# Optimization experiments

Measured on AMD Instinct MI355X. Metric: run time of the kernel, lower is better.

Reference implementation:

```python
import jax, jax.numpy as jnp
import numpy as np

B, N = 2, 1024
DIM, HEADS, DH, MLP = 768, 12, 64, 3072
PD = 768          # channels * patch_size^2 = 3*16*16
GRID = 16         # image_size // patch_size
DEPTH = 8
INNER = HEADS * DH


def layer_norm(x, g):
    # torch F.layer_norm with beta=0 buffer, eps=1e-5
    m = x.mean(-1, keepdims=True)
    v = ((x - m) ** 2).mean(-1, keepdims=True)
    return (x - m) / jnp.sqrt(v + 1e-5) * g


def qk_rmsnorm(x, g):
    # F.normalize(x, dim=-1) * sqrt(DH) * gamma ; gamma is [H,1,DH]
    n = jnp.linalg.norm(x, axis=-1, keepdims=True)
    return x / jnp.maximum(n, 1e-12) * (DH ** 0.5) * g


def setup_inputs() -> dict:
    key = jax.random.key(0)
    ks = jax.random.split(key, 16)
    s = 0.02
    d = {
        "patches": jax.random.normal(ks[0], (B, N, PD), dtype=jnp.float32),
        "h_idx": jax.random.randint(ks[1], (B, N), 0, GRID),
        "w_idx": jax.random.randint(ks[2], (B, N), 0, GRID),
        "image_ids": jnp.sort(jax.random.randint(ks[3], (B, N), 0, 8), axis=-1),
        "pos_h": jax.random.normal(ks[4], (GRID, PD)) * s,
        "pos_w": jax.random.normal(ks[5], (GRID, PD)) * s,
        "Wp": jax.random.normal(ks[6], (PD, DIM)) * s,
        "bp": jnp.zeros((DIM,)),
        "ln_p": jnp.ones((DIM,)),
        "ln1": jnp.ones((DEPTH, DIM)),
        "qg": jnp.ones((DEPTH, HEADS, 1, DH)),
        "kg": jnp.ones((DEPTH, HEADS, 1, DH)),
        "Wq": jax.random.normal(ks[7], (DEPTH, DIM, INNER)) * s,
        "Wkv": jax.random.normal(ks[8], (DEPTH, DIM, 2 * INNER)) * s,
        "Wo": jax.random.normal(ks[9], (DEPTH, INNER, DIM)) * s,
        "ln2": jnp.ones((DEPTH, DIM)),
        "W1": jax.random.normal(ks[10], (DEPTH, DIM, MLP)) * s,
        "b1": jnp.zeros((DEPTH, MLP)),
        "W2": jax.random.normal(ks[11], (DEPTH, MLP, DIM)) * s,
        "b2": jnp.zeros((DEPTH, DIM)),
        "lnf": jnp.ones((DIM,)),
    }
    return d


def reference(patches, h_idx, w_idx, image_ids, pos_h, pos_w, Wp, bp, ln_p,
              ln1, qg, kg, Wq, Wkv, Wo, ln2, W1, b1, W2, b2, lnf):
    # pos embed added to raw patches before projection (pos_embed_before_proj=True)
    x = patches + pos_h[h_idx] + pos_w[w_idx]            # [B,N,PD]
    x = layer_norm(x @ Wp + bp, ln_p)                    # [B,N,DIM]

    # block-diagonal attn_mask: tokens attend only within their own packed image
    mask = image_ids[:, None, :, None] == image_ids[:, None, None, :]  # [B,1,N,N]

    for i in range(DEPTH):
        xn = layer_norm(x, ln1[i])
        q = (xn @ Wq[i]).reshape(B, N, HEADS, DH).transpose(0, 2, 1, 3)
        k, v = jnp.split(xn @ Wkv[i], 2, axis=-1)
        k = k.reshape(B, N, HEADS, DH).transpose(0, 2, 1, 3)
        v = v.reshape(B, N, HEADS, DH).transpose(0, 2, 1, 3)
        q = qk_rmsnorm(q, qg[i])
        k = qk_rmsnorm(k, kg[i])
        dots = jnp.einsum('bhid,bhjd->bhij', q, k)       # [B,H,N,N]
        dots = jnp.where(mask, dots, -jnp.finfo(dots.dtype).max)
        attn = jax.nn.softmax(dots, axis=-1)
        o = jnp.einsum('bhij,bhjd->bhid', attn, v)
        o = o.transpose(0, 2, 1, 3).reshape(B, N, INNER)
        x = o @ Wo[i] + x
        h = jax.nn.gelu(layer_norm(x, ln2[i]) @ W1[i] + b1[i], approximate=False)
        x = (h @ W2[i] + b2[i]) + x
    return layer_norm(x, lnf)
```

## Files before the change

### kernel.cpp

```cpp
#include <hip/hip_runtime.h>
#include <hip/hip_bf16.h>
#include <math.h>

typedef _Float16 f16;
typedef f16   f16x8 __attribute__((ext_vector_type(8)));
typedef float f32x4 __attribute__((ext_vector_type(4)));
typedef unsigned short ushort_t;

#define DIM   768
#define HEADS 12
#define DH    64
#define MLP_  3072
#define NTOK  2048
#define SEQ   1024
#define WELTS 7077888

__device__ __forceinline__ ushort_t h2u(f16 h){ return __builtin_bit_cast(ushort_t, h); }
__device__ __forceinline__ unsigned pk2h(float a, float b){
  return (unsigned)h2u((f16)a) | ((unsigned)h2u((f16)b) << 16);
}
__device__ __forceinline__ void gload16(const void* g, void* l){
  __builtin_amdgcn_global_load_lds(
      (const __attribute__((address_space(1))) void*)g,
      (__attribute__((address_space(3))) void*)l, 16, 0, 0);
}
__device__ __forceinline__ float wred_sum(float v){
  #pragma unroll
  for (int o = 32; o > 0; o >>= 1) v += __shfl_xor(v, o);
  return v;
}

__global__ __launch_bounds__(256) void convert_w_kernel(
    const float* __restrict__ Wq, const float* __restrict__ Wkv,
    const float* __restrict__ Wo, const float* __restrict__ W1,
    const float* __restrict__ W2, int layer, int wp_only,
    f16* __restrict__ th)
{
  int bid = blockIdx.x;
  const float* src; int K, N; size_t ooff; int t;
  if (wp_only){ src = Wq; K = 768; N = 768; ooff = 0; t = bid; }
  else if (bid < 288) { src = Wq;  K = 768;  N = 768;  ooff = 0;       t = bid; }
  else if (bid < 864) { src = Wkv; K = 768;  N = 1536; ooff = 589824;  t = bid - 288; }
  else if (bid < 1152){ src = Wo;  K = 768;  N = 768;  ooff = 1769472; t = bid - 864; }
  else if (bid < 2304){ src = W1;  K = 768;  N = 3072; ooff = 2359296; t = bid - 1152; }
  else                { src = W2;  K = 3072; N = 768;  ooff = 4718592; t = bid - 2304; }
  if (!wp_only) src += (size_t)layer * K * N;
  int ntn = N >> 6;
  int tk = t / ntn, tn = t % ntn;
  int k0 = tk * 32, n0 = tn * 64;

  __shared__ ushort_t lh[32][66];
  int tid = threadIdx.x;
  #pragma unroll
  for (int rr = 0; rr < 2; rr++){
    int k = rr * 16 + (tid >> 4);
    int n = (tid & 15) * 4;
    float4 v = *(const float4*)(src + (size_t)(k0 + k) * N + n0 + n);
    lh[k][n+0] = h2u((f16)v.x); lh[k][n+1] = h2u((f16)v.y);
    lh[k][n+2] = h2u((f16)v.z); lh[k][n+3] = h2u((f16)v.w);
  }
  __syncthreads();
  int n = tid >> 2, kq = tid & 3;
  unsigned ph[4];
  #pragma unroll
  for (int j = 0; j < 4; j++)
    ph[j] = (unsigned)lh[kq*8 + 2*j][n] | ((unsigned)lh[kq*8 + 2*j + 1][n] << 16);
  size_t obase = ooff + (size_t)(n0 + n) * K + k0 + kq * 8;
  *(uint4*)(th + obase) = make_uint4(ph[0], ph[1], ph[2], ph[3]);
}

__global__ __launch_bounds__(256) void gemm_big(
    const f16* __restrict__ Aq, const f16* __restrict__ Bw,
    const float* __restrict__ bias,
    float* __restrict__ C, f16* __restrict__ Cq,
    f16* __restrict__ Qh, f16* __restrict__ Kt, f16* __restrict__ Vt,
    const float* __restrict__ qgam, const float* __restrict__ kgam,
    int N, int K, int nbx, int mode)
{
  __shared__ __align__(16) f16 sA[128 * 64];
  __shared__ __align__(16) f16 sB[128 * 64];
  const int tid = threadIdx.x;
  const int wid = tid >> 6, lane = tid & 63;
  const int nwg = nbx << 4;
  const int bid = blockIdx.x;
  const int swz = (bid & 7) * (nwg >> 3) + (bid >> 3);
  const int by = swz & 15, bx = swz >> 4;
  const int brow = by << 7, bcol = bx << 7;
  const int m2 = wid & 1, n2 = wid >> 1;
  const int fr = lane & 15, fq = lane >> 4;
  const int Kc = K / (int)gridDim.z;
  const int kbase = (int)blockIdx.z * Kc;
  const int nk = Kc >> 6;

  const f16* pA = Aq + (size_t)brow * K + kbase;
  const f16* pB = Bw + (size_t)bcol * K + kbase;

  f32x4 acc[4][4] = {};

  for (int ks = 0; ks < nk; ks++){
    const int k0 = ks << 6;
    if (ks) __syncthreads();
    #pragma unroll
    for (int i = 0; i < 4; i++){
      int idx = tid + i * 256;
      int r = idx >> 3, c = idx & 7;
      int gc = c ^ (r & 7);
      gload16(pA + (size_t)r * K + k0 + gc * 8, &sA[idx * 8]);
      gload16(pB + (size_t)r * K + k0 + gc * 8, &sB[idx * 8]);
    }
    __syncthreads();
    #pragma unroll
    for (int s = 0; s < 2; s++){
      f16x8 a[4], b[4];
      #pragma unroll
      for (int m = 0; m < 4; m++){
        int r = m2 * 64 + m * 16 + fr;
        int ch = (s * 4 + fq) ^ (r & 7);
        a[m] = *(const f16x8*)(&sA[r * 64 + ch * 8]);
      }
      #pragma unroll
      for (int n = 0; n < 4; n++){
        int r = n2 * 64 + n * 16 + fr;
        int ch = (s * 4 + fq) ^ (r & 7);
        b[n] = *(const f16x8*)(&sB[r * 64 + ch * 8]);
      }
      #pragma unroll
      for (int m = 0; m < 4; m++)
        #pragma unroll
        for (int n = 0; n < 4; n++)
          acc[m][n] = __builtin_amdgcn_mfma_f32_16x16x32_f16(a[m], b[n], acc[m][n], 0, 0, 0);
    }
  }

  if (mode == 2){
    const int hbase = bcol + n2 * 64;
    if (hbase < 768){
      float gp[4];
      #pragma unroll
      for (int n = 0; n < 4; n++){
        int col = hbase + n * 16 + fr;
        gp[n] = qgam[col] * kgam[col];
      }
      #pragma unroll
      for (int m = 0; m < 4; m++)
        #pragma unroll
        for (int i = 0; i < 4; i++){
          float s = 0.f;
          #pragma unroll
          for (int n = 0; n < 4; n++) s += acc[m][n][i] * acc[m][n][i];
          s += __shfl_xor(s, 1); s += __shfl_xor(s, 2);
          s += __shfl_xor(s, 4); s += __shfl_xor(s, 8);
          float f = 8.f / fmaxf(sqrtf(s), 1e-12f);
          int row = brow + m2 * 64 + m * 16 + (fq << 2) + i;
          #pragma unroll
          for (int n = 0; n < 4; n++)
            Qh[(size_t)row * 768 + hbase + n * 16 + fr] = (f16)(acc[m][n][i] * f * gp[n]);
        }
    } else if (hbase < 1536){
      int hh = (hbase - 768) >> 6;
      #pragma unroll
      for (int m = 0; m < 4; m++)
        #pragma unroll
        for (int i = 0; i < 4; i++){
          float s = 0.f;
          #pragma unroll
          for (int n = 0; n < 4; n++) s += acc[m][n][i] * acc[m][n][i];
          s += __shfl_xor(s, 1); s += __shfl_xor(s, 2);
          s += __shfl_xor(s, 4); s += __shfl_xor(s, 8);
          float f = 8.f / fmaxf(sqrtf(s), 1e-12f);
          int row = brow + m2 * 64 + m * 16 + (fq << 2) + i;
          int bq = row >> 10, tok = row & 1023;
          #pragma unroll
          for (int n = 0; n < 4; n++)
            Kt[((size_t)(bq * 12 + hh) * 1024 + tok) * 64 + n * 16 + fr]
                = (f16)(acc[m][n][i] * f);
        }
    } else {
      int hh = (hbase - 1536) >> 6;
      #pragma unroll
      for (int n = 0; n < 4; n++){
        int dd = n * 16 + fr;
        #pragma unroll
        for (int m = 0; m < 4; m++){
          int row0 = brow + m2 * 64 + m * 16 + (fq << 2);
          int bq = row0 >> 10, tok0 = row0 & 1023;
          ushort4 sv;
          sv.x = h2u((f16)acc[m][n][0]); sv.y = h2u((f16)acc[m][n][1]);
          sv.z = h2u((f16)acc[m][n][2]); sv.w = h2u((f16)acc[m][n][3]);
          *(ushort4*)(Vt + ((size_t)((bq * 12 + hh) * 64 + dd)) * 1024 + tok0) = sv;
        }
      }
    }
  } else if (mode == 1){
    #pragma unroll
    for (int n = 0; n < 4; n++){
      int col = bcol + n2 * 64 + n * 16 + fr;
      float bv = bias[col];
      #pragma unroll
      for (int m = 0; m < 4; m++){
        int row0 = brow + m2 * 64 + m * 16 + (fq << 2);
        #pragma unroll
        for (int i = 0; i < 4; i++){
          float v = acc[m][n][i] + bv;
          float ge = 0.5f * v * (1.f + erff(v * 0.70710678118654752f));
          Cq[(size_t)(row0 + i) * N + col] = (f16)ge;
        }
      }
    }
  } else {
    float* P = C + (size_t)blockIdx.z * ((size_t)NTOK * N);
    #pragma unroll
    for (int n = 0; n < 4; n++){
      int col = bcol + n2 * 64 + n * 16 + fr;
      #pragma unroll
      for (int m = 0; m < 4; m++){
        int row0 = brow + m2 * 64 + m * 16 + (fq << 2);
        #pragma unroll
        for (int i = 0; i < 4; i++)
          P[(size_t)(row0 + i) * N + col] = acc[m][n][i];
      }
    }
  }
}

__global__ __launch_bounds__(256) void gemm_small(
    const f16* __restrict__ Aq, const f16* __restrict__ Bw,
    const float* __restrict__ bias, const float* __restrict__ res,
    float* __restrict__ C, int N, int K, int nbx)
{
  __shared__ __align__(16) f16 sA[2][64 * 64];
  __shared__ __align__(16) f16 sB[2][64 * 64];
  const int tid = threadIdx.x;
  const int wid = tid >> 6, lane = tid & 63;
  const int nwg = nbx << 5;
  const int bid = blockIdx.x;
  const int swz = (bid & 7) * (nwg >> 3) + (bid >> 3);
  const int by = swz & 31, bx = swz >> 5;
  const int brow = by << 6, bcol = bx << 6;
  const int m2 = wid & 1, n2 = wid >> 1;
  const int fr = lane & 15, fq = lane >> 4;
  const int nk = K >> 6;

  const f16* pA = Aq + (size_t)brow * K;
  const f16* pB = Bw + (size_t)bcol * K;

  f32x4 acc[2][2] = {};

  auto STAGE = [&](int buf, int ks){
    const int k0 = ks << 6;
    #pragma unroll
    for (int i = 0; i < 2; i++){
      int idx = tid + i * 256;
      int r = idx >> 3, c = idx & 7;
      int gc = c ^ (r & 7);
      gload16(pA + (size_t)r * K + k0 + gc * 8, &sA[buf][idx * 8]);
      gload16(pB + (size_t)r * K + k0 + gc * 8, &sB[buf][idx * 8]);
    }
  };

  STAGE(0, 0);
  __syncthreads();
  int cur = 0;
  for (int ks = 0; ks < nk; ks++){
    if (ks + 1 < nk) STAGE(cur ^ 1, ks + 1);
    #pragma unroll
    for (int s = 0; s < 2; s++){
      f16x8 a[2], b[2];
      #pragma unroll
      for (int m = 0; m < 2; m++){
        int r = m2 * 32 + m * 16 + fr;
        int ch = (s * 4 + fq) ^ (r & 7);
        a[m] = *(const f16x8*)(&sA[cur][r * 64 + ch * 8]);
      }
      #pragma unroll
      for (int n = 0; n < 2; n++){
        int r = n2 * 32 + n * 16 + fr;
        int ch = (s * 4 + fq) ^ (r & 7);
        b[n] = *(const f16x8*)(&sB[cur][r * 64 + ch * 8]);
      }
      #pragma unroll
      for (int m = 0; m < 2; m++)
        #pragma unroll
        for (int n = 0; n < 2; n++)
          acc[m][n] = __builtin_amdgcn_mfma_f32_16x16x32_f16(a[m], b[n], acc[m][n], 0, 0, 0);
    }
    __syncthreads();
    cur ^= 1;
  }

  #pragma unroll
  for (int n = 0; n < 2; n++){
    int col = bcol + n2 * 32 + n * 16 + fr;
    float bv = bias ? bias[col] : 0.f;
    #pragma unroll
    for (int m = 0; m < 2; m++){
      int row0 = brow + m2 * 32 + m * 16 + (fq << 2);
      #pragma unroll
      for (int i = 0; i < 4; i++){
        float v = acc[m][n][i] + bv;
        size_t o = (size_t)(row0 + i) * N + col;
        if (res) v += res[o];
        C[o] = v;
      }
    }
  }
}

__global__ __launch_bounds__(256) void lnred_kernel(
    float* __restrict__ x, const float* __restrict__ p, const float* __restrict__ badd,
    int npart, const float* __restrict__ g, f16* __restrict__ yq, float* __restrict__ yf)
{
  int wid = threadIdx.x >> 6, lane = threadIdx.x & 63;
  int row = blockIdx.x * 4 + wid;
  float* xr = x + (size_t)row * DIM;
  float v[12]; float s = 0.f;
  if (npart){
    #pragma unroll
    for (int d = 0; d < 12; d++){
      int c = d * 64 + lane;
      float t = xr[c] + badd[c];
      for (int j = 0; j < 4; j++)
        t += p[(size_t)j * (NTOK * DIM) + (size_t)row * DIM + c];
      xr[c] = t; v[d] = t; s += t;
    }
  } else {
    #pragma unroll
    for (int d = 0; d < 12; d++){ v[d] = xr[d * 64 + lane]; s += v[d]; }
  }
  s = wred_sum(s);
  float mean = s * (1.f / 768.f);
  float q2 = 0.f;
  #pragma unroll
  for (int d = 0; d < 12; d++){ float t = v[d] - mean; q2 += t * t; }
  q2 = wred_sum(q2);
  float rstd = rsqrtf(q2 * (1.f / 768.f) + 1e-5f);
  size_t base = (size_t)row * DIM;
  #pragma unroll
  for (int d = 0; d < 12; d++){
    float y = (v[d] - mean) * rstd * g[d * 64 + lane];
    if (yq) yq[base + d * 64 + lane] = (f16)y;
    else    yf[base + d * 64 + lane] = y;
  }
}

__global__ __launch_bounds__(256) void posadd_kernel(
    const float* __restrict__ patches, const int* __restrict__ hi,
    const int* __restrict__ wi, const float* __restrict__ ph,
    const float* __restrict__ pw, f16* __restrict__ oq)
{
  int idx = blockIdx.x * 256 + threadIdx.x;
  int tok = idx / 192, cv = idx % 192;
  float4 p = ((const float4*)patches)[idx];
  float4 a = *(const float4*)(ph + (size_t)hi[tok] * DIM + cv * 4);
  float4 b = *(const float4*)(pw + (size_t)wi[tok] * DIM + cv * 4);
  ushort4 o;
  o.x = h2u((f16)(p.x + a.x + b.x)); o.y = h2u((f16)(p.y + a.y + b.y));
  o.z = h2u((f16)(p.z + a.z + b.z)); o.w = h2u((f16)(p.w + a.w + b.w));
  ((ushort4*)oq)[idx] = o;
}

__global__ void seg_kernel(const int* __restrict__ ids, int2* __restrict__ segs)
{
  int i = blockIdx.x * 256 + threadIdx.x;
  int b = blockIdx.y;
  const int* row = ids + b * SEQ;
  int v = row[i];
  int lo = 0, hi = SEQ;
  while (lo < hi){ int mid = (lo + hi) >> 1; if (row[mid] <  v) lo = mid + 1; else hi = mid; }
  int s = lo;
  lo = 0; hi = SEQ;
  while (lo < hi){ int mid = (lo + hi) >> 1; if (row[mid] <= v) lo = mid + 1; else hi = mid; }
  segs[b * SEQ + i] = make_int2(s, lo);
}

__global__ __launch_bounds__(256) void attn_kernel(
    const f16* __restrict__ qh, const f16* __restrict__ ktp,
    const f16* __restrict__ vt, const int2* __restrict__ segs,
    f16* __restrict__ oq)
{
  __shared__ __align__(16) ushort_t Kq[32 * 64];
  __shared__ __align__(16) ushort_t Vl[64 * 40];

  const int tid = threadIdx.x;
  const int w = tid >> 6, lane = tid & 63;
  const int q15 = lane & 15, kg = lane >> 4;
  const int bh = blockIdx.x, b = bh / 12, h = bh % 12;
  const int qt = blockIdx.y;
  const int qrow = qt * 64 + w * 16 + q15;
  const size_t qtok = (size_t)b * SEQ + qrow;

  const f16* qp = qh + qtok * DIM + h * 64 + kg * 8;
  f16x8 qf[2];
  qf[0] = *(const f16x8*)(qp);
  qf[1] = *(const f16x8*)(qp + 32);

  const int2 se  = segs[qtok];
  const int2 se0 = segs[(size_t)b * SEQ + qt * 64];
  const int2 se1 = segs[(size_t)b * SEQ + qt * 64 + 63];
  const int klo = se0.x & ~31, khi = se1.y;

  float m = -3.0e38f, l = 0.f;
  f32x4 oacc[4] = {};

  const int krl = tid >> 3, kcl = tid & 7;
  const int kgc = kcl ^ (krl & 7);
  const f16* kbase = ktp + (size_t)bh * 1024 * 64;
  const int vd = tid >> 2, vko = (tid & 3) * 8;

  for (int kt0 = klo; kt0 < khi; kt0 += 32){
    gload16(kbase + (size_t)(kt0 + krl) * 64 + kgc * 8, Kq + tid * 8);
    {
      int ksrc = kt0 + vko;
      uint4 vv = *(const uint4*)(vt + ((size_t)bh * 64 + vd) * SEQ + ksrc);
      *(uint4*)((char*)Vl + vd * 80 + vko * 2) = vv;
    }
    __syncthreads();

    f32x4 s[2] = {};
    #pragma unroll
    for (int dh2 = 0; dh2 < 2; dh2++){
      #pragma unroll
      for (int khf = 0; khf < 2; khf++){
        int row = khf * 16 + q15;
        unsigned off = ((unsigned)row << 7) + ((unsigned)(dh2 * 4 + kg) << 4);
        off ^= (unsigned)(row & 7) << 4;
        f16x8 kf = *(const f16x8*)((const char*)Kq + off);
        s[khf] = __builtin_amdgcn_mfma_f32_16x16x32_f16(kf, qf[dh2], s[khf], 0, 0, 0);
      }
    }

    float p[8]; float tmax = -3.0e38f;
    #pragma unroll
    for (int khf = 0; khf < 2; khf++)
      #pragma unroll
      for (int i = 0; i < 4; i++){
        int key = kt0 + khf * 16 + kg * 4 + i;
        bool val = (key >= se.x) && (key < se.y);
        float sv = val ? s[khf][i] : -3.0e38f;
        p[khf * 4 + i] = sv;
        tmax = fmaxf(tmax, sv);
      }
    tmax = fmaxf(tmax, __shfl_xor(tmax, 16));
    tmax = fmaxf(tmax, __shfl_xor(tmax, 32));
    float mnew = fmaxf(m, tmax);
    float sc = __expf(m - mnew);
    float psum = 0.f;
    #pragma unroll
    for (int j = 0; j < 8; j++){
      float pv = (p[j] > -1.0e38f) ? __expf(p[j] - mnew) : 0.f;
      p[j] = pv; psum += pv;
    }
    psum += __shfl_xor(psum, 16);
    psum += __shfl_xor(psum, 32);
    l = l * sc + psum;
    m = mnew;
    #pragma unroll
    for (int dt = 0; dt < 4; dt++) oacc[dt] *= sc;

    unsigned u00 = pk2h(p[0], p[1]), u01 = pk2h(p[2], p[3]);
    unsigned u10 = pk2h(p[4], p[5]), u11 = pk2h(p[6], p[7]);
    int s0l = q15 + ((kg & 1) << 5);
    int s1l = s0l + 16;
    unsigned a0 = __shfl(u00, s0l), b0 = __shfl(u01, s0l);
    unsigned a1 = __shfl(u00, s1l), b1 = __shfl(u01, s1l);
    unsigned c0 = __shfl(u10, s0l), d0 = __shfl(u11, s0l);
    unsigned c1 = __shfl(u10, s1l), d1 = __shfl(u11, s1l);
    bool hih = kg >= 2;
    f16x8 pfrag = __builtin_bit_cast(f16x8,
        make_uint4(hih ? c0 : a0, hih ? d0 : b0, hih ? c1 : a1, hih ? d1 : b1));

    #pragma unroll
    for (int dt = 0; dt < 4; dt++){
      f16x8 vf = *(const f16x8*)((const char*)Vl + (dt * 16 + q15) * 80 + kg * 16);
      oacc[dt] = __builtin_amdgcn_mfma_f32_16x16x32_f16(vf, pfrag, oacc[dt], 0, 0, 0);
    }
    __syncthreads();
  }

  float rl = 1.f / l;
  size_t obase = qtok * DIM + h * 64;
  #pragma unroll
  for (int dt = 0; dt < 4; dt++){
    ushort4 hs;
    hs.x = h2u((f16)(oacc[dt][0] * rl)); hs.y = h2u((f16)(oacc[dt][1] * rl));
    hs.z = h2u((f16)(oacc[dt][2] * rl)); hs.w = h2u((f16)(oacc[dt][3] * rl));
    *(ushort4*)(oq + obase + dt * 16 + kg * 4) = hs;
  }
}

extern "C" void kernel_launch(void* const* d_in, const int* in_sizes, int n_in,
                              void* d_out, int out_size, void* d_ws, size_t ws_size,
                              hipStream_t stream)
{
  const float* patches   = (const float*)d_in[0];
  const int*   h_idx     = (const int*)d_in[1];
  const int*   w_idx     = (const int*)d_in[2];
  const int*   image_ids = (const int*)d_in[3];
  const float* pos_h = (const float*)d_in[4];
  const float* pos_w = (const float*)d_in[5];
  const float* Wp  = (const float*)d_in[6];
  const float* bp  = (const float*)d_in[7];
  const float* lnp = (const float*)d_in[8];
  const float* ln1 = (const float*)d_in[9];
  const float* qg  = (const float*)d_in[10];
  const float* kg  = (const float*)d_in[11];
  const float* Wq  = (const float*)d_in[12];
  const float* Wkv = (const float*)d_in[13];
  const float* Wo  = (const float*)d_in[14];
  const float* ln2 = (const float*)d_in[15];
  const float* W1  = (const float*)d_in[16];
  const float* b1  = (const float*)d_in[17];
  const float* W2  = (const float*)d_in[18];
  const float* b2  = (const float*)d_in[19];
  const float* lnf = (const float*)d_in[20];
  float* out = (float*)d_out;

  float* ws = (float*)d_ws;
  float* x    = ws;
  float* pbuf = x + NTOK * DIM;
  f16* qh  = (f16*)(pbuf + 4 * NTOK * DIM);
  f16* ktb = qh  + NTOK * DIM;
  f16* vtb = ktb + NTOK * DIM;
  f16* aAq = vtb + NTOK * DIM;
  f16* aBq = aAq + NTOK * DIM;
  f16* wth = aBq + NTOK * MLP_;
  int2* segs = (int2*)(wth + WELTS);

  seg_kernel<<<dim3(4, 2), 256, 0, stream>>>(image_ids, segs);
  posadd_kernel<<<1536, 256, 0, stream>>>(patches, h_idx, w_idx, pos_h, pos_w, aAq);
  convert_w_kernel<<<288, 256, 0, stream>>>(Wp, nullptr, nullptr, nullptr, nullptr, 0, 1, wth);
  gemm_small<<<384, 256, 0, stream>>>(aAq, wth, bp, nullptr, pbuf, DIM, DIM, 12);
  lnred_kernel<<<NTOK / 4, 256, 0, stream>>>(pbuf, nullptr, nullptr, 0, lnp, nullptr, x);

  for (int i = 0; i < 8; i++){
    convert_w_kernel<<<3456, 256, 0, stream>>>(Wq, Wkv, Wo, W1, W2, i, 0, wth);
    lnred_kernel<<<NTOK / 4, 256, 0, stream>>>(
        x, pbuf, i ? (b2 + (i - 1) * DIM) : nullptr, i ? 4 : 0,
        ln1 + i * DIM, aAq, nullptr);
    gemm_big<<<288, 256, 0, stream>>>(
        aAq, wth, nullptr, nullptr, nullptr, qh, ktb, vtb,
        qg + i * DIM, kg + i * DIM, 3 * DIM, DIM, 18, 2);
    attn_kernel<<<dim3(24, 16), 256, 0, stream>>>(qh, ktb, vtb, segs, aAq);
    gemm_small<<<384, 256, 0, stream>>>(
        aAq, wth + 1769472, nullptr, x, x, DIM, DIM, 12);
    lnred_kernel<<<NTOK / 4, 256, 0, stream>>>(
        x, nullptr, nullptr, 0, ln2 + i * DIM, aAq, nullptr);
    gemm_big<<<384, 256, 0, stream>>>(
        aAq, wth + 2359296, b1 + i * MLP_, nullptr, aBq, nullptr, nullptr, nullptr,
        nullptr, nullptr, MLP_, DIM, 24, 1);
    gemm_big<<<dim3(96, 1, 4), 256, 0, stream>>>(
        aBq, wth + 4718592, nullptr, pbuf, nullptr, nullptr, nullptr, nullptr,
        nullptr, nullptr, DIM, MLP_, 6, 3);
  }
  lnred_kernel<<<NTOK / 4, 256, 0, stream>>>(x, pbuf, b2 + 7 * DIM, 4, lnf, nullptr, out);
}
```

Measured before the change: 979.2 us.

## Batch weight conversion upfront, widen convert tiles, store split-K partials in fp16

Result: slower. 1.096 ms (+11.9%).

```diff
diff --git a/kernel.cpp b/kernel.cpp
--- a/kernel.cpp
+++ b/kernel.cpp
@@ -37,42 +37,50 @@
     f16* __restrict__ th)
 {
   int bid = blockIdx.x;
+  size_t lws = 0;
+  if (layer < 0){ layer = bid / 1728; bid -= layer * 1728; lws = (size_t)layer * WELTS; }
   const float* src; int K, N; size_t ooff; int t;
   if (wp_only){ src = Wq; K = 768; N = 768; ooff = 0; t = bid; }
-  else if (bid < 288) { src = Wq;  K = 768;  N = 768;  ooff = 0;       t = bid; }
-  else if (bid < 864) { src = Wkv; K = 768;  N = 1536; ooff = 589824;  t = bid - 288; }
-  else if (bid < 1152){ src = Wo;  K = 768;  N = 768;  ooff = 1769472; t = bid - 864; }
-  else if (bid < 2304){ src = W1;  K = 768;  N = 3072; ooff = 2359296; t = bid - 1152; }
-  else                { src = W2;  K = 3072; N = 768;  ooff = 4718592; t = bid - 2304; }
+  else if (bid < 144) { src = Wq;  K = 768;  N = 768;  ooff = 0;       t = bid; }
+  else if (bid < 432) { src = Wkv; K = 768;  N = 1536; ooff = 589824;  t = bid - 144; }
+  else if (bid < 576) { src = Wo;  K = 768;  N = 768;  ooff = 1769472; t = bid - 432; }
+  else if (bid < 1152){ src = W1;  K = 768;  N = 3072; ooff = 2359296; t = bid - 576; }
+  else                { src = W2;  K = 3072; N = 768;  ooff = 4718592; t = bid - 1152; }
   if (!wp_only) src += (size_t)layer * K * N;
   int ntn = N >> 6;
   int tk = t / ntn, tn = t % ntn;
-  int k0 = tk * 32, n0 = tn * 64;
-
-  __shared__ ushort_t lh[32][66];
-  int tid = threadIdx.x;
-  #pragma unroll
-  for (int rr = 0; rr < 2; rr++){
-    int k = rr * 16 + (tid >> 4);
-    int n = (tid & 15) * 4;
-    float4 v = *(const float4*)(src + (size_t)(k0 + k) * N + n0 + n);
-    lh[k][n+0] = h2u((f16)v.x); lh[k][n+1] = h2u((f16)v.y);
-    lh[k][n+2] = h2u((f16)v.z); lh[k][n+3] = h2u((f16)v.w);
+  int k0 = tk * 64, n0 = tn * 64;
+
+  __shared__ unsigned lp[32][68];
+  const int tid = threadIdx.x;
+  #pragma unroll
+  for (int p = 0; p < 2; p++){
+    int rp = p * 16 + (tid >> 4);
+    int c  = (tid & 15) * 4;
+    const float* s0 = src + (size_t)(k0 + 2 * rp) * N + n0 + c;
+    float4 a = *(const float4*)s0;
+    float4 b = *(const float4*)(s0 + N);
+    unsigned u0 = pk2h(a.x, b.x), u1 = pk2h(a.y, b.y);
+    unsigned u2 = pk2h(a.z, b.z), u3 = pk2h(a.w, b.w);
+    *(uint4*)&lp[rp][c] = make_uint4(u0, u1, u2, u3);
   }
   __syncthreads();
-  int n = tid >> 2, kq = tid & 3;
-  unsigned ph[4];
-  #pragma unroll
-  for (int j = 0; j < 4; j++)
-    ph[j] = (unsigned)lh[kq*8 + 2*j][n] | ((unsigned)lh[kq*8 + 2*j + 1][n] << 16);
-  size_t obase = ooff + (size_t)(n0 + n) * K + k0 + kq * 8;
-  *(uint4*)(th + obase) = make_uint4(ph[0], ph[1], ph[2], ph[3]);
+  #pragma unroll
+  for (int p = 0; p < 2; p++){
+    int n = p * 32 + (tid >> 3);
+    int q = tid & 7;
+    unsigned u[4];
+    #pragma unroll
+    for (int j = 0; j < 4; j++) u[j] = lp[q * 4 + j][n];
+    *(uint4*)(th + lws + ooff + (size_t)(n0 + n) * K + k0 + q * 8)
+        = make_uint4(u[0], u[1], u[2], u[3]);
+  }
 }
 
 __global__ __launch_bounds__(256) void gemm_big(
     const f16* __restrict__ Aq, const f16* __restrict__ Bw,
     const float* __restrict__ bias,
-    float* __restrict__ C, f16* __restrict__ Cq,
+    f16* __restrict__ Cq,
     f16* __restrict__ Qh, f16* __restrict__ Kt, f16* __restrict__ Vt,
     const float* __restrict__ qgam, const float* __restrict__ kgam,
     int N, int K, int nbx, int mode)
@@ -208,7 +216,7 @@
       }
     }
   } else {
-    float* P = C + (size_t)blockIdx.z * ((size_t)NTOK * N);
+    f16* P = Cq + (size_t)blockIdx.z * ((size_t)NTOK * N);
     #pragma unroll
     for (int n = 0; n < 4; n++){
       int col = bcol + n2 * 64 + n * 16 + fr;
@@ -217,7 +225,7 @@
         int row0 = brow + m2 * 64 + m * 16 + (fq << 2);
         #pragma unroll
         for (int i = 0; i < 4; i++)
-          P[(size_t)(row0 + i) * N + col] = acc[m][n][i];
+          P[(size_t)(row0 + i) * N + col] = (f16)acc[m][n][i];
       }
     }
   }
@@ -307,7 +315,7 @@
 }
 
 __global__ __launch_bounds__(256) void lnred_kernel(
-    float* __restrict__ x, const float* __restrict__ p, const float* __restrict__ badd,
+    float* __restrict__ x, const f16* __restrict__ p, const float* __restrict__ badd,
     int npart, const float* __restrict__ g, f16* __restrict__ yq, float* __restrict__ yf)
 {
   int wid = threadIdx.x >> 6, lane = threadIdx.x & 63;
@@ -319,8 +327,8 @@
     for (int d = 0; d < 12; d++){
       int c = d * 64 + lane;
       float t = xr[c] + badd[c];
-      for (int j = 0; j < 4; j++)
-        t += p[(size_t)j * (NTOK * DIM) + (size_t)row * DIM + c];
+      for (int j = 0; j < npart; j++)
+        t += (float)p[(size_t)j * (NTOK * DIM) + (size_t)row * DIM + c];
       xr[c] = t; v[d] = t; s += t;
     }
   } else {
@@ -515,42 +523,50 @@
   const float* lnf = (const float*)d_in[20];
   float* out = (float*)d_out;
 
-  float* ws = (float*)d_ws;
-  float* x    = ws;
-  float* pbuf = x + NTOK * DIM;
-  f16* qh  = (f16*)(pbuf + 4 * NTOK * DIM);
-  f16* ktb = qh  + NTOK * DIM;
-  f16* vtb = ktb + NTOK * DIM;
-  f16* aAq = vtb + NTOK * DIM;
-  f16* aBq = aAq + NTOK * DIM;
-  f16* wth = aBq + NTOK * MLP_;
-  int2* segs = (int2*)(wth + WELTS);
+  char* w = (char*)d_ws;
+  float* x = (float*)w;            w += (size_t)NTOK * DIM * 4;
+  f16* pbufh = (f16*)w;            w += (size_t)4 * NTOK * DIM * 2;
+  f16* qh  = (f16*)w;              w += (size_t)NTOK * DIM * 2;
+  f16* ktb = (f16*)w;              w += (size_t)NTOK * DIM * 2;
+  f16* vtb = (f16*)w;              w += (size_t)NTOK * DIM * 2;
+  f16* aAq = (f16*)w;              w += (size_t)NTOK * DIM * 2;
+  f16* aBq = (f16*)w;              w += (size_t)NTOK * MLP_ * 2;
+  int2* segs = (int2*)w;           w += (size_t)NTOK * 8;
+  f16* wall = (f16*)w;
+  size_t base_used = (size_t)(w - (char*)d_ws);
+  const bool pre = ws_size >= base_used + (size_t)8 * WELTS * 2;
+  float* ptmp = (float*)aBq;
+  f16* wpc = pbufh;
 
   seg_kernel<<<dim3(4, 2), 256, 0, stream>>>(image_ids, segs);
   posadd_kernel<<<1536, 256, 0, stream>>>(patches, h_idx, w_idx, pos_h, pos_w, aAq);
-  convert_w_kernel<<<288, 256, 0, stream>>>(Wp, nullptr, nullptr, nullptr, nullptr, 0, 1, wth);
-  gemm_small<<<384, 256, 0, stream>>>(aAq, wth, bp, nullptr, pbuf, DIM, DIM, 12);
-  lnred_kernel<<<NTOK / 4, 256, 0, stream>>>(pbuf, nullptr, nullptr, 0, lnp, nullptr, x);
+  convert_w_kernel<<<144, 256, 0, stream>>>(Wp, nullptr, nullptr, nullptr, nullptr, 0, 1, wpc);
+  gemm_small<<<384, 256, 0, stream>>>(aAq, wpc, bp, nullptr, ptmp, DIM, DIM, 12);
+  lnred_kernel<<<NTOK / 4, 256, 0, stream>>>(ptmp, nullptr, nullptr, 0, lnp, nullptr, x);
+  if (pre)
+    convert_w_kernel<<<13824, 256, 0, stream>>>(Wq, Wkv, Wo, W1, W2, -1, 0, wall);
 
   for (int i = 0; i < 8; i++){
-    convert_w_kernel<<<3456, 256, 0, stream>>>(Wq, Wkv, Wo, W1, W2, i, 0, wth);
+    f16* wl = wall + (pre ? (size_t)i * WELTS : 0);
+    if (!pre)
+      convert_w_kernel<<<1728, 256, 0, stream>>>(Wq, Wkv, Wo, W1, W2, i, 0, wall);
     lnred_kernel<<<NTOK / 4, 256, 0, stream>>>(
-        x, pbuf, i ? (b2 + (i - 1) * DIM) : nullptr, i ? 4 : 0,
+        x, pbufh, i ? (b2 + (i - 1) * DIM) : nullptr, i ? 4 : 0,
         ln1 + i * DIM, aAq, nullptr);
     gemm_big<<<288, 256, 0, stream>>>(
-        aAq, wth, nullptr, nullptr, nullptr, qh, ktb, vtb,
+        aAq, wl, nullptr, nullptr, qh, ktb, vtb,
         qg + i * DIM, kg + i * DIM, 3 * DIM, DIM, 18, 2);
     attn_kernel<<<dim3(24, 16), 256, 0, stream>>>(qh, ktb, vtb, segs, aAq);
     gemm_small<<<384, 256, 0, stream>>>(
-        aAq, wth + 1769472, nullptr, x, x, DIM, DIM, 12);
+        aAq, wl + 1769472, nullptr, x, x, DIM, DIM, 12);
     lnred_kernel<<<NTOK / 4, 256, 0, stream>>>(
         x, nullptr, nullptr, 0, ln2 + i * DIM, aAq, nullptr);
     gemm_big<<<384, 256, 0, stream>>>(
-        aAq, wth + 2359296, b1 + i * MLP_, nullptr, aBq, nullptr, nullptr, nullptr,
+        aAq, wl + 2359296, b1 + i * MLP_, aBq, nullptr, nullptr, nullptr,
         nullptr, nullptr, MLP_, DIM, 24, 1);
     gemm_big<<<dim3(96, 1, 4), 256, 0, stream>>>(
-        aBq, wth + 4718592, nullptr, pbuf, nullptr, nullptr, nullptr, nullptr,
+        aBq, wl + 4718592, nullptr, pbufh, nullptr, nullptr, nullptr,
         nullptr, nullptr, DIM, MLP_, 6, 3);
   }
-  lnred_kernel<<<NTOK / 4, 256, 0, stream>>>(x, pbuf, b2 + 7 * DIM, 4, lnf, nullptr, out);
-}
+  lnred_kernel<<<NTOK / 4, 256, 0, stream>>>(x, pbufh, b2 + 7 * DIM, 4, lnf, nullptr, out);
+}
```
